# Kernel tuning notes

Measured on AMD Instinct MI355X. Metric: run time of the kernel, lower is better.

## Reference

```python
import jax, jax.numpy as jnp
import numpy as np
import math

D_MODEL = 1024
N_HEAD = 16
D_HEAD = D_MODEL // N_HEAD
B, T = 4, 2048


def setup_inputs() -> dict:
    key = jax.random.key(0)
    ks = jax.random.split(key, 9)
    x = jax.random.normal(ks[0], (B, T, D_MODEL), dtype=jnp.float32)
    # causal mask, broadcastable to [B, H, T, T]; mask==0 -> -1e9
    mask = jnp.tril(jnp.ones((T, T), dtype=bool))[None, None, :, :]
    # Xavier-uniform linear weights (stored as [in, out] for x @ W), zero biases
    limit = math.sqrt(6.0 / (D_MODEL + D_MODEL))
    def w(k):
        return jax.random.uniform(k, (D_MODEL, D_MODEL), dtype=jnp.float32, minval=-limit, maxval=limit)
    return {
        "x": x,
        "mask": mask,
        "wq": w(ks[1]), "bq": jnp.zeros((D_MODEL,), jnp.float32),
        "wk": w(ks[2]), "bk": jnp.zeros((D_MODEL,), jnp.float32),
        "wv": w(ks[3]), "bv": jnp.zeros((D_MODEL,), jnp.float32),
        "wo": w(ks[4]), "bo": jnp.zeros((D_MODEL,), jnp.float32),
    }


def reference(x, mask, wq, bq, wk, bk, wv, bv, wo, bo):
    b, t, c = x.shape
    h, dh = N_HEAD, D_HEAD
    # [B,T,C] -> [B,H,T,dh]
    def heads(y):
        return y.reshape(b, t, h, dh).transpose(0, 2, 1, 3)
    q = heads(x @ wq + bq)
    k = heads(x @ wk + bk)
    v = heads(x @ wv + bv)
    att = jnp.einsum("bhqd,bhkd->bhqk", q, k) / math.sqrt(dh)
    att = jnp.where(mask, att, jnp.float32(-1e9))
    att = jax.nn.softmax(att, axis=-1)  # dropout is identity in eval mode
    out = jnp.einsum("bhqk,bhkd->bhqd", att, v)
    out = out.transpose(0, 2, 1, 3).reshape(b, t, c)
    return out @ wo + bo
```

## Files before the change

kernel.cpp:

```cpp
#include <hip/hip_runtime.h>

typedef __bf16 bf16_t;
typedef bf16_t bf16x8 __attribute__((ext_vector_type(8)));
typedef bf16_t bf16x4 __attribute__((ext_vector_type(4)));
typedef float  f32x4  __attribute__((ext_vector_type(4)));
typedef float  f32x16 __attribute__((ext_vector_type(16)));
typedef unsigned int u32;
typedef u32 u32x2 __attribute__((ext_vector_type(2)));
typedef u32 u32x4 __attribute__((ext_vector_type(4)));

#define T_SEQ 2048
#define C_DIM 1024
#define NH    16
#define DH    64
#define BATCH 4
#define M_TOK (BATCH * T_SEQ)

#define Q_SCALE 0.1803368801111137f
#define DEFER_THR 8.0f

#define AS1 __attribute__((address_space(1)))
#define AS3 __attribute__((address_space(3)))

__device__ __forceinline__ void gld_lds16(const bf16_t* g, bf16_t* l) {
  __builtin_amdgcn_global_load_lds(
      (const AS1 u32*)(uintptr_t)g,
      (AS3 u32*)(u32)(uintptr_t)l, 16, 0, 0);
}

__device__ __forceinline__ void plswap(u32& a, u32& b) {
  u32x2 r = __builtin_amdgcn_permlane32_swap(a, b, false, false);
  a = r[0]; b = r[1];
}
__device__ __forceinline__ float xmax32(float x) {
  u32 a = __builtin_bit_cast(u32, x), b = a;
  plswap(a, b);
  return fmaxf(__builtin_bit_cast(float, a), __builtin_bit_cast(float, b));
}
__device__ __forceinline__ float xsum32(float x) {
  u32 a = __builtin_bit_cast(u32, x), b = a;
  plswap(a, b);
  return __builtin_bit_cast(float, a) + __builtin_bit_cast(float, b);
}

__device__ __forceinline__ u32 pack_bf16_pair(float v0, float v1) {
  const unsigned short b0 = __builtin_bit_cast(unsigned short, (bf16_t)v0);
  const unsigned short b1 = __builtin_bit_cast(unsigned short, (bf16_t)v1);
  return ((u32)b1 << 16) | (u32)b0;
}

__global__ __launch_bounds__(256) void msa_prep(
    const float* __restrict__ x, bf16_t* __restrict__ xb,
    const float* __restrict__ wq, const float* __restrict__ wk,
    const float* __restrict__ wv, const float* __restrict__ wo,
    bf16_t* __restrict__ wt_qkv, bf16_t* __restrict__ wt_o) {
  __shared__ float tile[32][33];
  const int blk = blockIdx.x;
  if (blk < 8192) {
    const int i = blk * 256 + threadIdx.x;
    const float4 v = ((const float4*)x)[i];
    bf16x4 o;
    o[0] = (bf16_t)v.x; o[1] = (bf16_t)v.y; o[2] = (bf16_t)v.z; o[3] = (bf16_t)v.w;
    ((bf16x4*)xb)[i] = o;
  } else {
    const int b2 = blk - 8192;
    const int a = b2 >> 10;
    const int bx = b2 & 31, by = (b2 >> 5) & 31;
    const float* src = (a == 0) ? wq : (a == 1) ? wk : (a == 2) ? wv : wo;
    bf16_t* dst = (a < 3) ? (wt_qkv + (size_t)a * C_DIM * C_DIM) : wt_o;
    const int tx = threadIdx.x & 31, ty = threadIdx.x >> 5;
    const int bi = by * 32, bj = bx * 32;
#pragma unroll
    for (int p = 0; p < 4; p++) {
      int r = p * 8 + ty;
      tile[r][tx] = src[(size_t)(bi + r) * C_DIM + bj + tx];
    }
    __syncthreads();
#pragma unroll
    for (int p = 0; p < 4; p++) {
      int r = p * 8 + ty;
      dst[(size_t)(bj + r) * C_DIM + bi + tx] = (bf16_t)tile[tx][r];
    }
  }
}

#define GQ_BUF 24576

#define GEMM_CORE(APTR, BPTR, NT)                                              \
  __shared__ __align__(16) char lds[3 * GQ_BUF];                               \
  const int tid = threadIdx.x;                                                 \
  const int w = tid >> 6, lane = tid & 63;                                     \
  const int lr = lane & 15, lg = lane >> 4;                                    \
  const int m0 = blockIdx.y * 256;                                             \
  const int n0 = blockIdx.x * 128;                                             \
  const int wm = (w >> 1) * 64, wn = (w & 1) * 64;                             \
  const int rsw = (lg * 16) ^ ((lr & 3) << 4);                                 \
  int Aoff[4], Boff[4];                                                        \
  _Pragma("unroll") for (int f = 0; f < 4; f++) {                              \
    Aoff[f] = (wm + f * 16 + lr) * 64 + rsw;                                   \
    Boff[f] = 16384 + (wn + f * 16 + lr) * 64 + rsw;                           \
  }                                                                            \
  const int srow = tid >> 2;                                                   \
  const int scol = (((tid & 3) ^ (srow & 3))) * 8;                             \
  const bf16_t* gA0 = (APTR) + (size_t)(m0 + srow) * C_DIM + scol;             \
  const bf16_t* gA1 = (APTR) + (size_t)(m0 + 128 + srow) * C_DIM + scol;       \
  const bf16_t* gB0 = (BPTR) + (size_t)(n0 + srow) * C_DIM + scol;             \
  f32x4 acc[4][4];                                                             \
  _Pragma("unroll") for (int i = 0; i < 4; i++)                                \
    _Pragma("unroll") for (int j = 0; j < 4; j++)                              \
      acc[i][j] = (f32x4){0.f, 0.f, 0.f, 0.f};                                 \
  GSTG(0, 0);                                                                  \
  GSTG(1, GQ_BUF);                                                             \
  asm volatile("s_waitcnt vmcnt(3)" ::: "memory");                             \
  __builtin_amdgcn_s_barrier();                                                \
  __builtin_amdgcn_sched_barrier(0);                                           \
  int cb = 0;                                                                  \
  for (int kt = 0; kt < (NT); ++kt) {                                          \
    const char* base = lds + cb * GQ_BUF;                                      \
    bf16x8 a[4], b[4];                                                         \
    _Pragma("unroll") for (int f = 0; f < 4; f++) {                            \
      a[f] = *(const bf16x8*)(base + Aoff[f]);                                 \
      b[f] = *(const bf16x8*)(base + Boff[f]);                                 \
    }                                                                          \
    if (kt < (NT)-2) {                                                         \
      int sb = cb + 2; if (sb >= 3) sb -= 3;                                   \
      GSTG(kt + 2, sb * GQ_BUF);                                               \
    }                                                                          \
    __builtin_amdgcn_s_setprio(1);                                             \
    _Pragma("unroll") for (int mf = 0; mf < 4; mf++)                           \
      _Pragma("unroll") for (int nf = 0; nf < 4; nf++)                         \
        acc[mf][nf] = __builtin_amdgcn_mfma_f32_16x16x32_bf16(                 \
            a[mf], b[nf], acc[mf][nf], 0, 0, 0);                               \
    __builtin_amdgcn_s_setprio(0);                                             \
    if (kt < (NT)-2) {                                                         \
      asm volatile("s_waitcnt vmcnt(3)" ::: "memory");                         \
    } else {                                                                   \
      asm volatile("s_waitcnt vmcnt(0)" ::: "memory");                         \
    }                                                                          \
    __builtin_amdgcn_s_barrier();                                              \
    __builtin_amdgcn_sched_barrier(0);                                         \
    if (++cb == 3) cb = 0;                                                     \
  }

#define GSTG(KT, BB)                                                           \
  {                                                                            \
    bf16_t* d_ = (bf16_t*)(lds + (BB));                                        \
    gld_lds16(gA0 + (KT) * 32, d_ + tid * 8);                                  \
    gld_lds16(gA1 + (KT) * 32, d_ + 4096 + tid * 8);                           \
    gld_lds16(gB0 + (KT) * 32, d_ + 8192 + tid * 8);                           \
  }

__global__ __launch_bounds__(512, 4) void msa_gemm_qkv(
    const bf16_t* __restrict__ xb, const bf16_t* __restrict__ wt,
    const float* __restrict__ bq, const float* __restrict__ bk,
    const float* __restrict__ bv,
    bf16_t* __restrict__ qo, bf16_t* __restrict__ ko, bf16_t* __restrict__ vto) {
  GEMM_CORE(xb, wt, 32)

  const int g = n0 >> 10;
  if (g == 2) {
#pragma unroll
    for (int nb = 0; nb < 4; nb++) {
      const int c = ((n0 + wn) & 1023) + nb * 16 + lr;
      const int h = c >> 6, d = c & 63;
      const float bias = bv[c];
      bf16_t* vrow = vto + (((size_t)((m0 >> 11) * NH + h)) * DH + d) * T_SEQ;
#pragma unroll
      for (int mb = 0; mb < 4; mb++) {
        const int t = (m0 & 2047) + wm + mb * 16 + lg * 4;
        u32x2 pr;
        pr[0] = pack_bf16_pair(acc[mb][nb][0] + bias, acc[mb][nb][1] + bias);
        pr[1] = pack_bf16_pair(acc[mb][nb][2] + bias, acc[mb][nb][3] + bias);
        *reinterpret_cast<u32x2*>(vrow + t) = pr;
      }
    }
  } else {
#pragma unroll
    for (int nb = 0; nb < 4; nb++) {
      const int n = n0 + wn + nb * 16 + lr;
      const int c = n & 1023, h = c >> 6, d = c & 63;
      const float bias = (g == 0) ? bq[c] : bk[c];
#pragma unroll
      for (int mb = 0; mb < 4; mb++) {
#pragma unroll
        for (int r = 0; r < 4; r++) {
          const int m = m0 + wm + mb * 16 + lg * 4 + r;
          const int bi = m >> 11, t = m & (T_SEQ - 1);
          float v = acc[mb][nb][r] + bias;
          if (g == 0)
            qo[(((size_t)bi * NH + h) * T_SEQ + t) * DH + d] = (bf16_t)(v * Q_SCALE);
          else
            ko[(((size_t)bi * NH + h) * T_SEQ + t) * DH + d] = (bf16_t)v;
        }
      }
    }
  }
}

__global__ __launch_bounds__(512, 4) void msa_gemm_out(
    const bf16_t* __restrict__ ab, const bf16_t* __restrict__ wt,
    const float* __restrict__ bo, float* __restrict__ out) {
  GEMM_CORE(ab, wt, 32)

#pragma unroll
  for (int nb = 0; nb < 4; nb++) {
    const int n = n0 + wn + nb * 16 + lr;
    const float bias = bo[n];
#pragma unroll
    for (int mb = 0; mb < 4; mb++) {
#pragma unroll
      for (int r = 0; r < 4; r++) {
        const int m = m0 + wm + mb * 16 + lg * 4 + r;
        out[(size_t)m * C_DIM + n] = acc[mb][nb][r] + bias;
      }
    }
  }
}

__device__ __forceinline__ void pack_frag(const f32x16& s, bf16x8& pa0, bf16x8& pa1) {
  u32 pk8[8];
#pragma unroll
  for (int i = 0; i < 8; i++) pk8[i] = pack_bf16_pair(s[2 * i], s[2 * i + 1]);
  u32 f0w0 = pk8[0], f0w2 = pk8[2];
  u32 f0w1 = pk8[1], f0w3 = pk8[3];
  u32 f1w0 = pk8[4], f1w2 = pk8[6];
  u32 f1w1 = pk8[5], f1w3 = pk8[7];
  plswap(f0w0, f0w2);
  plswap(f0w1, f0w3);
  plswap(f1w0, f1w2);
  plswap(f1w1, f1w3);
  const u32x4 q0v = {f0w0, f0w1, f0w2, f0w3};
  const u32x4 q1v = {f1w0, f1w1, f1w2, f1w3};
  pa0 = __builtin_bit_cast(bf16x8, q0v);
  pa1 = __builtin_bit_cast(bf16x8, q1v);
}

__device__ __forceinline__ void sm_pack(f32x16& s, float& m_run, float& l_run,
                                        f32x16& o0, f32x16& o1,
                                        bf16x8& pa0, bf16x8& pa1) {
  float t0 = fmaxf(fmaxf(s[0], s[1]), s[2]);
  float t1 = fmaxf(fmaxf(s[3], s[4]), s[5]);
  float t2 = fmaxf(fmaxf(s[6], s[7]), s[8]);
  float t3 = fmaxf(fmaxf(s[9], s[10]), s[11]);
  float t4 = fmaxf(fmaxf(s[12], s[13]), s[14]);
  float t5 = fmaxf(fmaxf(t0, t1), s[15]);
  float mt = fmaxf(fmaxf(fmaxf(t2, t3), t4), t5);
  mt = xmax32(mt);

  if (__any(mt > m_run + DEFER_THR)) {
    const float mnew = fmaxf(m_run, mt);
    const float al = __builtin_amdgcn_exp2f(m_run - mnew);
    m_run = mnew;
    l_run *= al;
#pragma unroll
    for (int r = 0; r < 16; r++) { o0[r] *= al; o1[r] *= al; }
  }

#pragma unroll
  for (int r = 0; r < 16; r++) s[r] = __builtin_amdgcn_exp2f(s[r] - m_run);
  {
    float a0 = (s[0] + s[1]) + (s[2] + s[3]);
    float a1 = (s[4] + s[5]) + (s[6] + s[7]);
    float a2 = (s[8] + s[9]) + (s[10] + s[11]);
    float a3 = (s[12] + s[13]) + (s[14] + s[15]);
    l_run += xsum32((a0 + a1) + (a2 + a3));
  }
  pack_frag(s, pa0, pa1);
}

__device__ __forceinline__ void store_o(f32x16& o0, f32x16& o1, float l_fin,
                                        bf16_t* __restrict__ orow, const int hi) {
  const float inv = 1.0f / l_fin;
#pragma unroll
  for (int db = 0; db < 2; db++) {
#pragma unroll
    for (int r = 0; r < 16; r += 2) {
      const int d = db * 32 + (r & 3) + 8 * (r >> 2) + 4 * hi;
      const float v0 = (db ? o1[r] : o0[r]) * inv;
      const float v1 = (db ? o1[r + 1] : o0[r + 1]) * inv;
      *reinterpret_cast<u32*>(orow + d) = pack_bf16_pair(v0, v1);
    }
  }
}

__global__ __launch_bounds__(256, 2) void msa_attn_lds(
    const bf16_t* __restrict__ Q, const bf16_t* __restrict__ K,
    const bf16_t* __restrict__ Vt, bf16_t* __restrict__ O) {
  __shared__ __align__(16) char lds[16384];
  const int tid = threadIdx.x;
  const int w = tid >> 6;
  const int lane = tid & 63;
  const int l31 = lane & 31;
  const int hi = lane >> 5;
  const int bh = blockIdx.x;
  const int pg = blockIdx.y;
  const int p = pg * 4 + w;
  const int tS = p, tL = 63 - p;
  const int q0S = tS * 32, q0L = tL * 32;
  const int KT_MAX = 63 - 4 * pg;

  const bf16_t* Qh = Q + (size_t)bh * T_SEQ * DH;
  const bf16_t* Kh = K + (size_t)bh * T_SEQ * DH;
  const bf16_t* Vh = Vt + (size_t)bh * DH * T_SEQ;

  bf16x8 qfL[4], qfS[4];
#pragma unroll
  for (int dc = 0; dc < 4; dc++) {
    qfL[dc] = *(const bf16x8*)(Qh + (size_t)(q0L + l31) * DH + dc * 16 + hi * 8);
    qfS[dc] = *(const bf16x8*)(Qh + (size_t)(q0S + l31) * DH + dc * 16 + hi * 8);
  }

  f32x16 oL0, oL1, oS0, oS1;
#pragma unroll
  for (int r = 0; r < 16; r++) { oL0[r] = 0.f; oL1[r] = 0.f; oS0[r] = 0.f; oS1[r] = 0.f; }
  float mL = -1e30f, lL = 0.f, mS = -1e30f, lS = 0.f;
  const f32x16 z16 = {};

  const int ksw = (l31 & 7) << 4;
  const int vsw = (l31 & 3) << 4;
  const int krow = tid >> 3;
  const int kce = ((16 * (tid & 7)) ^ ((krow & 7) << 4)) >> 1;
  const int vrow = tid >> 2;
  const int vce = ((16 * (tid & 3)) ^ ((vrow & 3) << 4)) >> 1;

#define STAGE(KT, BUF)                                                         \
  {                                                                            \
    const int jj = (KT) * 32;                                                  \
    bf16_t* base_ = (bf16_t*)(lds + (BUF) * 8192);                             \
    gld_lds16(Kh + (size_t)(jj + krow) * DH + kce, base_ + tid * 8);           \
    gld_lds16(Vh + (size_t)vrow * T_SEQ + jj + vce, base_ + 2048 + tid * 8);   \
  }

  STAGE(0, 0);
  __syncthreads();

  for (int kt = 0; kt <= KT_MAX; ++kt) {
    const int buf = kt & 1;
    if (kt < KT_MAX) STAGE(kt + 1, buf ^ 1);

    const bool doL = (kt <= tL);
    if (doL) {
      const char* kb = lds + buf * 8192;
      const char* vb = kb + 4096;
      bf16x8 kf[4];
#pragma unroll
      for (int dc = 0; dc < 4; dc++)
        kf[dc] = *(const bf16x8*)(kb + l31 * 128 + ((dc * 32 + hi * 16) ^ ksw));
      const bf16x8 vf00 = *(const bf16x8*)(vb + l31 * 64 + ((hi * 16) ^ vsw));
      const bf16x8 vf01 = *(const bf16x8*)(vb + l31 * 64 + ((32 + hi * 16) ^ vsw));
      const bf16x8 vf10 = *(const bf16x8*)(vb + (32 + l31) * 64 + ((hi * 16) ^ vsw));
      const bf16x8 vf11 = *(const bf16x8*)(vb + (32 + l31) * 64 + ((32 + hi * 16) ^ vsw));

      const bool doS = (kt <= tS);
      f32x16 sL = __builtin_amdgcn_mfma_f32_32x32x16_bf16(kf[0], qfL[0], z16, 0, 0, 0);
#pragma unroll
      for (int dc = 1; dc < 4; dc++)
        sL = __builtin_amdgcn_mfma_f32_32x32x16_bf16(kf[dc], qfL[dc], sL, 0, 0, 0);
      f32x16 sS;
      if (doS) {
        sS = __builtin_amdgcn_mfma_f32_32x32x16_bf16(kf[0], qfS[0], z16, 0, 0, 0);
#pragma unroll
        for (int dc = 1; dc < 4; dc++)
          sS = __builtin_amdgcn_mfma_f32_32x32x16_bf16(kf[dc], qfS[dc], sS, 0, 0, 0);
      }
      if (kt == tL) {
#pragma unroll
        for (int r = 0; r < 16; r++) {
          const int jrow = (r & 3) + 8 * (r >> 2) + 4 * hi;
          if (jrow > l31) sL[r] = -1e30f;
        }
      }
      if (kt == tS) {
#pragma unroll
        for (int r = 0; r < 16; r++) {
          const int jrow = (r & 3) + 8 * (r >> 2) + 4 * hi;
          if (jrow > l31) sS[r] = -1e30f;
        }
      }
      bf16x8 paL0, paL1;
      sm_pack(sL, mL, lL, oL0, oL1, paL0, paL1);
      oL0 = __builtin_amdgcn_mfma_f32_32x32x16_bf16(vf00, paL0, oL0, 0, 0, 0);
      oL1 = __builtin_amdgcn_mfma_f32_32x32x16_bf16(vf10, paL0, oL1, 0, 0, 0);
      oL0 = __builtin_amdgcn_mfma_f32_32x32x16_bf16(vf01, paL1, oL0, 0, 0, 0);
      oL1 = __builtin_amdgcn_mfma_f32_32x32x16_bf16(vf11, paL1, oL1, 0, 0, 0);
      if (doS) {
        bf16x8 paS0, paS1;
        sm_pack(sS, mS, lS, oS0, oS1, paS0, paS1);
        oS0 = __builtin_amdgcn_mfma_f32_32x32x16_bf16(vf00, paS0, oS0, 0, 0, 0);
        oS1 = __builtin_amdgcn_mfma_f32_32x32x16_bf16(vf10, paS0, oS1, 0, 0, 0);
        oS0 = __builtin_amdgcn_mfma_f32_32x32x16_bf16(vf01, paS1, oS0, 0, 0, 0);
        oS1 = __builtin_amdgcn_mfma_f32_32x32x16_bf16(vf11, paS1, oS1, 0, 0, 0);
      }
    }
    __syncthreads();
  }
#undef STAGE

  const int b = bh >> 4, h = bh & 15;
  store_o(oL0, oL1, lL, O + ((size_t)b * T_SEQ + q0L + l31) * C_DIM + h * DH, hi);
  store_o(oS0, oS1, lS, O + ((size_t)b * T_SEQ + q0S + l31) * C_DIM + h * DH, hi);
}

extern "C" void kernel_launch(void* const* d_in, const int* in_sizes, int n_in,
                              void* d_out, int out_size, void* d_ws, size_t ws_size,
                              hipStream_t stream) {
  const float* x  = (const float*)d_in[0];
  const float* wq = (const float*)d_in[2];
  const float* bq = (const float*)d_in[3];
  const float* wk = (const float*)d_in[4];
  const float* bk = (const float*)d_in[5];
  const float* wv = (const float*)d_in[6];
  const float* bv = (const float*)d_in[7];
  const float* wo = (const float*)d_in[8];
  const float* bo = (const float*)d_in[9];

  char* ws = (char*)d_ws;
  bf16_t* xb     = (bf16_t*)(ws);
  bf16_t* wt_qkv = (bf16_t*)(ws + (16ull << 20));
  bf16_t* wt_o   = (bf16_t*)(ws + (22ull << 20));
  bf16_t* qb     = (bf16_t*)(ws + (24ull << 20));
  bf16_t* kb     = (bf16_t*)(ws + (40ull << 20));
  bf16_t* vtb    = (bf16_t*)(ws + (56ull << 20));
  bf16_t* attn_o = xb;

  msa_prep<<<12288, 256, 0, stream>>>(x, xb, wq, wk, wv, wo, wt_qkv, wt_o);
  msa_gemm_qkv<<<dim3(24, 32), 512, 0, stream>>>(xb, wt_qkv, bq, bk, bv, qb, kb, vtb);
  msa_attn_lds<<<dim3(64, 8), 256, 0, stream>>>(qb, kb, vtb, attn_o);
  msa_gemm_out<<<dim3(8, 32), 512, 0, stream>>>(attn_o, wt_o, bo, (float*)d_out);
}
```

Measured before the change: 161.2 us.

## Process 64-key blocks per iteration with joint softmax over two KV tiles

The attention loop now stages two 32-key K/V tiles per iteration into a doubled LDS buffer and computes both QK tiles before one shared online-softmax update over 64 keys. This halves the number of loop iterations and __syncthreads barriers and amortizes the max/rescale reductions across twice the keys. In exchange it doubles LDS use per block to 32KB and raises register pressure, which may limit occupancy under launch_bounds(256,2). K/V fragments are now reloaded from LDS separately for the long and short query streams rather than shared.

After: 161.8 us. About the same (+0.4%).

```diff
diff --git a/kernel.cpp b/kernel.cpp
--- a/kernel.cpp
+++ b/kernel.cpp
@@ -268,6 +268,47 @@
   pack_frag(s, pa0, pa1);
 }
 
+__device__ __forceinline__ void sm_pack64(f32x16& s0, f32x16& s1,
+                                          float& m_run, float& l_run,
+                                          f32x16& o0, f32x16& o1,
+                                          bf16x8& a0, bf16x8& a1,
+                                          bf16x8& b0, bf16x8& b1) {
+  float t[8];
+#pragma unroll
+  for (int i = 0; i < 8; i++)
+    t[i] = fmaxf(fmaxf(s0[2 * i], s0[2 * i + 1]), fmaxf(s1[2 * i], s1[2 * i + 1]));
+  float u0 = fmaxf(fmaxf(t[0], t[1]), t[2]);
+  float u1 = fmaxf(fmaxf(t[3], t[4]), t[5]);
+  float mt = fmaxf(fmaxf(fmaxf(t[6], t[7]), u0), u1);
+  mt = xmax32(mt);
+
+  if (__any(mt > m_run + DEFER_THR)) {
+    const float mnew = fmaxf(m_run, mt);
+    const float al = __builtin_amdgcn_exp2f(m_run - mnew);
+    m_run = mnew;
+    l_run *= al;
+#pragma unroll
+    for (int r = 0; r < 16; r++) { o0[r] *= al; o1[r] *= al; }
+  }
+
+#pragma unroll
+  for (int r = 0; r < 16; r++) {
+    s0[r] = __builtin_amdgcn_exp2f(s0[r] - m_run);
+    s1[r] = __builtin_amdgcn_exp2f(s1[r] - m_run);
+  }
+  {
+    float a = 0.f, b = 0.f;
+#pragma unroll
+    for (int r = 0; r < 16; r += 4) {
+      a += (s0[r] + s0[r + 1]) + (s0[r + 2] + s0[r + 3]);
+      b += (s1[r] + s1[r + 1]) + (s1[r + 2] + s1[r + 3]);
+    }
+    l_run += xsum32(a + b);
+  }
+  pack_frag(s0, a0, a1);
+  pack_frag(s1, b0, b1);
+}
+
 __device__ __forceinline__ void store_o(f32x16& o0, f32x16& o1, float l_fin,
                                         bf16_t* __restrict__ orow, const int hi) {
   const float inv = 1.0f / l_fin;
@@ -283,10 +324,68 @@
   }
 }
 
+__device__ __forceinline__ void mask_diag(f32x16& s, int l31, int hi) {
+#pragma unroll
+  for (int r = 0; r < 16; r++) {
+    const int jrow = (r & 3) + 8 * (r >> 2) + 4 * hi;
+    if (jrow > l31) s[r] = -1e30f;
+  }
+}
+
+__device__ __forceinline__ f32x16 qk_tile(const char* kb, const bf16x8* qf,
+                                          int l31, int hi, int ksw,
+                                          const f32x16& z16) {
+  bf16x8 kf[4];
+#pragma unroll
+  for (int dc = 0; dc < 4; dc++)
+    kf[dc] = *(const bf16x8*)(kb + l31 * 128 + ((dc * 32 + hi * 16) ^ ksw));
+  f32x16 s = __builtin_amdgcn_mfma_f32_32x32x16_bf16(kf[0], qf[0], z16, 0, 0, 0);
+#pragma unroll
+  for (int dc = 1; dc < 4; dc++)
+    s = __builtin_amdgcn_mfma_f32_32x32x16_bf16(kf[dc], qf[dc], s, 0, 0, 0);
+  return s;
+}
+
+__device__ __forceinline__ void pv_tile(const char* vb, const bf16x8 pa0,
+                                        const bf16x8 pa1, int l31, int hi,
+                                        int vsw, f32x16& o0, f32x16& o1) {
+  const bf16x8 vf00 = *(const bf16x8*)(vb + l31 * 64 + ((hi * 16) ^ vsw));
+  const bf16x8 vf01 = *(const bf16x8*)(vb + l31 * 64 + ((32 + hi * 16) ^ vsw));
+  const bf16x8 vf10 = *(const bf16x8*)(vb + (32 + l31) * 64 + ((hi * 16) ^ vsw));
+  const bf16x8 vf11 = *(const bf16x8*)(vb + (32 + l31) * 64 + ((32 + hi * 16) ^ vsw));
+  o0 = __builtin_amdgcn_mfma_f32_32x32x16_bf16(vf00, pa0, o0, 0, 0, 0);
+  o1 = __builtin_amdgcn_mfma_f32_32x32x16_bf16(vf10, pa0, o1, 0, 0, 0);
+  o0 = __builtin_amdgcn_mfma_f32_32x32x16_bf16(vf01, pa1, o0, 0, 0, 0);
+  o1 = __builtin_amdgcn_mfma_f32_32x32x16_bf16(vf11, pa1, o1, 0, 0, 0);
+}
+
+__device__ __forceinline__ void do_stream64(const char* buf, int k0, int t,
+                                            const bf16x8* qf, float& m, float& l,
+                                            f32x16& o0, f32x16& o1, int l31,
+                                            int hi, int ksw, int vsw,
+                                            const f32x16& z16) {
+  if (k0 > t) return;
+  f32x16 s0 = qk_tile(buf, qf, l31, hi, ksw, z16);
+  const int k1 = k0 + 1;
+  if (k1 <= t) {
+    f32x16 s1 = qk_tile(buf + 8192, qf, l31, hi, ksw, z16);
+    if (k1 == t) mask_diag(s1, l31, hi);
+    bf16x8 a0, a1, b0, b1;
+    sm_pack64(s0, s1, m, l, o0, o1, a0, a1, b0, b1);
+    pv_tile(buf + 4096, a0, a1, l31, hi, vsw, o0, o1);
+    pv_tile(buf + 12288, b0, b1, l31, hi, vsw, o0, o1);
+  } else {
+    if (k0 == t) mask_diag(s0, l31, hi);
+    bf16x8 pa0, pa1;
+    sm_pack(s0, m, l, o0, o1, pa0, pa1);
+    pv_tile(buf + 4096, pa0, pa1, l31, hi, vsw, o0, o1);
+  }
+}
+
 __global__ __launch_bounds__(256, 2) void msa_attn_lds(
     const bf16_t* __restrict__ Q, const bf16_t* __restrict__ K,
     const bf16_t* __restrict__ Vt, bf16_t* __restrict__ O) {
-  __shared__ __align__(16) char lds[16384];
+  __shared__ __align__(16) char lds[2 * 16384];
   const int tid = threadIdx.x;
   const int w = tid >> 6;
   const int lane = tid & 63;
@@ -297,7 +396,7 @@
   const int p = pg * 4 + w;
   const int tS = p, tL = 63 - p;
   const int q0S = tS * 32, q0L = tL * 32;
-  const int KT_MAX = 63 - 4 * pg;
+  const int JP_MAX = 31 - 2 * pg;
 
   const bf16_t* Qh = Q + (size_t)bh * T_SEQ * DH;
   const bf16_t* Kh = K + (size_t)bh * T_SEQ * DH;
@@ -323,78 +422,30 @@
   const int vrow = tid >> 2;
   const int vce = ((16 * (tid & 3)) ^ ((vrow & 3) << 4)) >> 1;
 
-#define STAGE(KT, BUF)                                                         \
+#define STAGE2(JP, BUF)                                                        \
   {                                                                            \
-    const int jj = (KT) * 32;                                                  \
-    bf16_t* base_ = (bf16_t*)(lds + (BUF) * 8192);                             \
+    const int jj = (JP) * 64;                                                  \
+    bf16_t* base_ = (bf16_t*)(lds + (BUF) * 16384);                            \
     gld_lds16(Kh + (size_t)(jj + krow) * DH + kce, base_ + tid * 8);           \
     gld_lds16(Vh + (size_t)vrow * T_SEQ + jj + vce, base_ + 2048 + tid * 8);   \
-  }
-
-  STAGE(0, 0);
+    gld_lds16(Kh + (size_t)(jj + 32 + krow) * DH + kce, base_ + 4096 + tid * 8); \
+    gld_lds16(Vh + (size_t)vrow * T_SEQ + jj + 32 + vce, base_ + 6144 + tid * 8); \
+  }
+
+  STAGE2(0, 0);
   __syncthreads();
 
-  for (int kt = 0; kt <= KT_MAX; ++kt) {
-    const int buf = kt & 1;
-    if (kt < KT_MAX) STAGE(kt + 1, buf ^ 1);
-
-    const bool doL = (kt <= tL);
-    if (doL) {
-      const char* kb = lds + buf * 8192;
-      const char* vb = kb + 4096;
-      bf16x8 kf[4];
-#pragma unroll
-      for (int dc = 0; dc < 4; dc++)
-        kf[dc] = *(const bf16x8*)(kb + l31 * 128 + ((dc * 32 + hi * 16) ^ ksw));
-      const bf16x8 vf00 = *(const bf16x8*)(vb + l31 * 64 + ((hi * 16) ^ vsw));
-      const bf16x8 vf01 = *(const bf16x8*)(vb + l31 * 64 + ((32 + hi * 16) ^ vsw));
-      const bf16x8 vf10 = *(const bf16x8*)(vb + (32 + l31) * 64 + ((hi * 16) ^ vsw));
-      const bf16x8 vf11 = *(const bf16x8*)(vb + (32 + l31) * 64 + ((32 + hi * 16) ^ vsw));
-
-      const bool doS = (kt <= tS);
-      f32x16 sL = __builtin_amdgcn_mfma_f32_32x32x16_bf16(kf[0], qfL[0], z16, 0, 0, 0);
-#pragma unroll
-      for (int dc = 1; dc < 4; dc++)
-        sL = __builtin_amdgcn_mfma_f32_32x32x16_bf16(kf[dc], qfL[dc], sL, 0, 0, 0);
-      f32x16 sS;
-      if (doS) {
-        sS = __builtin_amdgcn_mfma_f32_32x32x16_bf16(kf[0], qfS[0], z16, 0, 0, 0);
-#pragma unroll
-        for (int dc = 1; dc < 4; dc++)
-          sS = __builtin_amdgcn_mfma_f32_32x32x16_bf16(kf[dc], qfS[dc], sS, 0, 0, 0);
-      }
-      if (kt == tL) {
-#pragma unroll
-        for (int r = 0; r < 16; r++) {
-          const int jrow = (r & 3) + 8 * (r >> 2) + 4 * hi;
-          if (jrow > l31) sL[r] = -1e30f;
-        }
-      }
-      if (kt == tS) {
-#pragma unroll
-        for (int r = 0; r < 16; r++) {
-          const int jrow = (r & 3) + 8 * (r >> 2) + 4 * hi;
-          if (jrow > l31) sS[r] = -1e30f;
-        }
-      }
-      bf16x8 paL0, paL1;
-      sm_pack(sL, mL, lL, oL0, oL1, paL0, paL1);
-      oL0 = __builtin_amdgcn_mfma_f32_32x32x16_bf16(vf00, paL0, oL0, 0, 0, 0);
-      oL1 = __builtin_amdgcn_mfma_f32_32x32x16_bf16(vf10, paL0, oL1, 0, 0, 0);
-      oL0 = __builtin_amdgcn_mfma_f32_32x32x16_bf16(vf01, paL1, oL0, 0, 0, 0);
-      oL1 = __builtin_amdgcn_mfma_f32_32x32x16_bf16(vf11, paL1, oL1, 0, 0, 0);
-      if (doS) {
-        bf16x8 paS0, paS1;
-        sm_pack(sS, mS, lS, oS0, oS1, paS0, paS1);
-        oS0 = __builtin_amdgcn_mfma_f32_32x32x16_bf16(vf00, paS0, oS0, 0, 0, 0);
-        oS1 = __builtin_amdgcn_mfma_f32_32x32x16_bf16(vf10, paS0, oS1, 0, 0, 0);
-        oS0 = __builtin_amdgcn_mfma_f32_32x32x16_bf16(vf01, paS1, oS0, 0, 0, 0);
-        oS1 = __builtin_amdgcn_mfma_f32_32x32x16_bf16(vf11, paS1, oS1, 0, 0, 0);
-      }
-    }
+  for (int jp = 0; jp <= JP_MAX; ++jp) {
+    const int buf = jp & 1;
+    if (jp < JP_MAX) STAGE2(jp + 1, buf ^ 1);
+
+    const char* bb = lds + buf * 16384;
+    const int k0 = 2 * jp;
+    do_stream64(bb, k0, tL, qfL, mL, lL, oL0, oL1, l31, hi, ksw, vsw, z16);
+    do_stream64(bb, k0, tS, qfS, mS, lS, oS0, oS1, l31, hi, ksw, vsw, z16);
     __syncthreads();
   }
-#undef STAGE
+#undef STAGE2
 
   const int b = bh >> 4, h = bh & 15;
   store_o(oL0, oL1, lL, O + ((size_t)b * T_SEQ + q0L + l31) * C_DIM + h * DH, hi);
```
